# Kernel optimization log

Hardware: AMD Instinct MI355X
Metric: run time of the kernel (lower is better)

The kernel has to match this reference:

```python
import jax, jax.numpy as jnp
import numpy as np

B, DIM, HEADS = 8, 1024, 8
DH = DIM // HEADS            # 128 = dim_head
MFEAT = 621                  # int(DH * log(DH)) performer features
MAXD = 4                     # max_rel_dist
IMG = 10                     # image side; source hardcodes stride 10 in scatter indices
L = IMG * IMG + 1            # geometry forces L = img_dim**2 + 1


def _geometry():
    m, K = MAXD, 2 * MAXD - 1
    base = np.arange(-m + 1, m)
    dx = np.broadcast_to(np.tile(base, K), (L, K * K))
    dy = np.broadcast_to(np.repeat(base, K), (L, K * K))
    x_off = np.concatenate([np.tile(np.arange(IMG), IMG), [0]])[:, None]
    y_off = np.concatenate([np.repeat(np.arange(IMG), IMG), [IMG]])[:, None]
    x_pos, y_pos = dx + x_off, dy + y_off
    diffs = np.abs(dx) + np.abs(dy)
    valid = (x_pos >= 0) & (x_pos < IMG) & (y_pos >= 0) & (y_pos < IMG) & (diffs < m)
    diffs = np.where(valid, diffs, m)  # invalid taps point at the max-dist encoding
    rel_window = (m - 1) * IMG + (m - 1)
    # scatter positions inside the unfold window (stride 10 hardcoded in source)
    indices = np.tile(np.arange(K), K) + np.repeat(np.arange(K) * 10, K)
    return jnp.asarray(diffs), jnp.asarray(valid), jnp.asarray(indices - rel_window)

DIFFS, VALID, OFFSETS = _geometry()  # [L,K2] int, [L,K2] bool, [K2] int


def softmax_kernel(data, proj, is_query, eps=1e-4):
    dn = data.shape[-1] ** -0.25
    ratio = proj.shape[0] ** -0.5
    dd = jnp.einsum('...id,jd->...ij', data * dn, proj)
    diag = (jnp.sum(data ** 2, -1) * (0.5 * dn * dn))[..., None]
    mx = jnp.max(dd, -1, keepdims=True) if is_query else jnp.max(dd)
    return ratio * (jnp.exp(dd - diag - mx) + eps)


def relative_attention(q, rpe, v):
    # q: [b,h,L,MFEAT] kernel features, rpe: [R,MFEAT], v: [b,h,L,DH]
    mde = rpe[-1]                                   # max-distance encoding
    v_sum = v.sum(-2)                               # [b,h,DH]
    q_dot = jnp.einsum('bhlm,rm->bhlr', q, rpe - mde)
    q_rel = jnp.take_along_axis(q_dot, DIFFS[None, None], axis=-1)  # [b,h,L,K2]
    q_rel = jnp.where(VALID[None, None], q_rel, 0.0)
    # gather v at relative offsets (equivalent to the zero-padded unfold +
    # sparse scatter of q_rel in the source, without the dense 67-wide window)
    pos = jnp.arange(L)[:, None] + OFFSETS[None, :]  # [L,K2]
    inb = (pos >= 0) & (pos < L)
    v_g = v[:, :, jnp.clip(pos, 0, L - 1), :]        # [b,h,L,K2,DH]
    v_g = jnp.where(inb[None, None, :, :, None], v_g, 0.0)
    denom = (rpe[DIFFS] - mde).sum(1) + mde * L      # [L,MFEAT]
    D_inv = 1.0 / jnp.einsum('bhlm,lm->bhl', q, denom)
    q_md = jnp.einsum('bhlm,m->bhl', q, mde)
    out = jnp.einsum('bhl,bhd->bhld', q_md, v_sum) + jnp.einsum('bhlk,bhlkd->bhld', q_rel, v_g)
    return out * D_inv[..., None]


def setup_inputs() -> dict:
    key = jax.random.key(0)
    ks = jax.random.split(key, 9)
    s = DIM ** -0.5
    return {
        'x': jax.random.normal(ks[0], (B, L, DIM), jnp.float32),
        'Wq': jax.random.normal(ks[1], (DIM, DIM), jnp.float32) * s,
        'bq': jnp.zeros((DIM,), jnp.float32),
        'Wv': jax.random.normal(ks[2], (DIM, DIM), jnp.float32) * s,
        'bv': jnp.zeros((DIM,), jnp.float32),
        'rpe': jax.random.normal(ks[3], (MAXD + 1, DH), jnp.float32) * 0.02,
        'proj': jax.random.normal(ks[4], (MFEAT, DH), jnp.float32),
        'Wo': jax.random.normal(ks[5], (DIM, DIM), jnp.float32) * s,
        'bo': jnp.zeros((DIM,), jnp.float32),
    }


def reference(x, Wq, bq, Wv, bv, rpe, proj, Wo, bo):
    b = x.shape[0]
    q = (x @ Wq.T + bq).reshape(b, L, HEADS, DH).transpose(0, 2, 1, 3)
    v = (x @ Wv.T + bv).reshape(b, L, HEADS, DH).transpose(0, 2, 1, 3)
    qf = softmax_kernel(q, proj, is_query=True)
    rf = softmax_kernel(rpe[None, None], proj, is_query=False)[0, 0]
    out = relative_attention(qf, rf, v)          # [b,h,L,DH]
    out = out.transpose(0, 2, 1, 3).reshape(b, L, DIM)
    return out @ Wo.T + bo
```

## Files before the change

kernel.cpp:

```cpp
#include <hip/hip_runtime.h>
#include <math.h>

namespace {

typedef __bf16 bf16_t;
typedef bf16_t bf16x8 __attribute__((ext_vector_type(8)));
typedef bf16_t bf16x4 __attribute__((ext_vector_type(4)));
typedef float f32x4 __attribute__((ext_vector_type(4)));

constexpr int B = 8, L = 101, DIM = 1024, H = 8, DH = 128, MF = 621, MFP = 640;
constexpr int BL = B * L;
constexpr int BLP = 832;
constexpr int BH = B * H;
constexpr int RR = BL * H;

constexpr float DN    = 0.29730177875068026f;
constexpr float DN2   = 0.08838834764831845f;
constexpr float RATIO = 0.04012861672f;
constexpr float EPS   = 1e-4f;

constexpr int NX = BL * DIM / 4;
constexpr int NP = MFP * 32;
constexpr int NR = 64 * DH / 4;
constexpr int NW = DIM * DIM / 4;
constexpr int NZ = 4 * (BLP - BL) * DIM / 4;
constexpr int NTOT = NX + NP + NR + 3 * NW + NZ;

__device__ __forceinline__ f32x4 mfma16(bf16x8 a, bf16x8 b, f32x4 c) {
  return __builtin_amdgcn_mfma_f32_16x16x32_bf16(a, b, c, 0, 0, 0);
}

__device__ __forceinline__ void split2(float f, bf16_t& h, bf16_t& l) {
  h = (bf16_t)f;
  l = (bf16_t)(f - (float)h);
}

__device__ __forceinline__ void gload_lds16(const bf16_t* g, bf16_t* l) {
  __builtin_amdgcn_global_load_lds(
      (const __attribute__((address_space(1))) void*)g,
      (__attribute__((address_space(3))) void*)l, 16, 0, 0);
}

__global__ __launch_bounds__(256) void split_all(const float* __restrict__ x,
                                                 const float* __restrict__ proj,
                                                 const float* __restrict__ rpe,
                                                 const float* __restrict__ Wq,
                                                 const float* __restrict__ Wv,
                                                 const float* __restrict__ Wo,
                                                 bf16_t* __restrict__ xh, bf16_t* __restrict__ xl,
                                                 bf16_t* __restrict__ ph,
                                                 bf16_t* __restrict__ rh, bf16_t* __restrict__ rl,
                                                 bf16_t* __restrict__ Wh,
                                                 bf16_t* __restrict__ Woh,
                                                 bf16_t* __restrict__ qh, bf16_t* __restrict__ ql) {
  const int u = blockIdx.x * 256 + threadIdx.x;
  if (u >= NTOT) return;
  auto emit2 = [](const float* s4, float sc, bf16_t* dh, bf16_t* dl, size_t off) {
    float4 f = *(const float4*)s4;
    bf16x4 hv, lv; bf16_t h, l;
    split2(f.x * sc, h, l); hv[0] = h; lv[0] = l;
    split2(f.y * sc, h, l); hv[1] = h; lv[1] = l;
    split2(f.z * sc, h, l); hv[2] = h; lv[2] = l;
    split2(f.w * sc, h, l); hv[3] = h; lv[3] = l;
    *(bf16x4*)(dh + off) = hv;
    *(bf16x4*)(dl + off) = lv;
  };
  auto emit1 = [](const float* s4, float sc, bf16_t* dh, size_t off) {
    float4 f = *(const float4*)s4;
    bf16x4 hv;
    hv[0] = (bf16_t)(f.x * sc); hv[1] = (bf16_t)(f.y * sc);
    hv[2] = (bf16_t)(f.z * sc); hv[3] = (bf16_t)(f.w * sc);
    *(bf16x4*)(dh + off) = hv;
  };
  int t = u;
  if (t < NX) { emit2(x + (size_t)t * 4, 1.f, xh, xl, (size_t)t * 4); return; }
  t -= NX;
  if (t < NP) {
    if ((t >> 5) < MF) emit1(proj + (size_t)t * 4, DN, ph, (size_t)t * 4);
    else { bf16x4 z = {}; *(bf16x4*)(ph + (size_t)t * 4) = z; }
    return;
  }
  t -= NP;
  if (t < NR) {
    if (t < 5 * DH / 4) emit2(rpe + (size_t)t * 4, 1.f, rh, rl, (size_t)t * 4);
    else { bf16x4 z = {}; *(bf16x4*)(rh + (size_t)t * 4) = z; *(bf16x4*)(rl + (size_t)t * 4) = z; }
    return;
  }
  t -= NR;
  if (t < NW) { emit1(Wq + (size_t)t * 4, 1.f, Wh, (size_t)t * 4); return; }
  t -= NW;
  if (t < NW) { emit1(Wv + (size_t)t * 4, 1.f, Wh, (size_t)(t + NW) * 4); return; }
  t -= NW;
  if (t < NW) { emit1(Wo + (size_t)t * 4, 1.f, Woh, (size_t)t * 4); return; }
  t -= NW;
  {
    const int buf = t / 6144, o = t % 6144;
    bf16_t* dst = (buf == 0) ? xh : (buf == 1) ? xl : (buf == 2) ? qh : ql;
    bf16x4 z = {};
    *(bf16x4*)(dst + (size_t)BL * DIM + (size_t)o * 4) = z;
  }
}

template<int MODE>
__global__ __launch_bounds__(256) void gemm64(const bf16_t* __restrict__ Ah,
                                              const bf16_t* __restrict__ Al,
                                              const bf16_t* __restrict__ Bh,
                                              const float* __restrict__ bias0,
                                              const float* __restrict__ bias1,
                                              float* __restrict__ Cf,
                                              bf16_t* __restrict__ Ch,
                                              bf16_t* __restrict__ Cl) {
  constexpr int K = 1024, BK = 64, NK = K / BK;
  __shared__ bf16_t lds[2][3][64 * 64];
  const int tid = threadIdx.x;
  const int w = tid >> 6, lane = tid & 63;
  const int wr = w >> 1, wc = w & 1;
  const int l15 = lane & 15, l4 = lane >> 4;
  const int rowBase = blockIdx.y * 64, colBase = blockIdx.x * 64;
  const int r8 = lane >> 3;
  const int cs = (lane & 7) ^ r8;
  const bf16_t* src = (w == 0) ? Ah : (w == 1) ? Al : Bh;
  const int grow0 = (w < 2) ? rowBase : colBase + ((w == 3) ? 32 : 0);
  const bf16_t* srcL = src + (size_t)(grow0 + r8) * K + cs * 8;
  const int tt = (w < 2) ? w : 2;
  const int dst0 = (w == 3) ? 32 * 64 : 0;
  auto STAGE = [&](int bf, int k0) {
    if (w < 2) {
#pragma unroll
      for (int j = 0; j < 8; ++j)
        gload_lds16(srcL + (size_t)(8 * j) * K + k0, &lds[bf][tt][j * 512]);
    } else {
#pragma unroll
      for (int j = 0; j < 4; ++j)
        gload_lds16(srcL + (size_t)(8 * j) * K + k0, &lds[bf][2][dst0 + j * 512]);
    }
  };
  const int ra0 = wr * 32 + l15, ra1 = ra0 + 16;
  const int rb0 = wc * 32 + l15, rb1 = rb0 + 16;
  auto TADDR = [](int row, int kg) { return row * 64 + (((kg) ^ (row & 7)) << 3); };
  f32x4 acc[2][2] = {};
  STAGE(0, 0);
  __syncthreads();
  int bf = 0;
  for (int ks = 0; ks < NK; ++ks) {
    if (ks + 1 < NK) STAGE(bf ^ 1, (ks + 1) * BK);
#pragma unroll
    for (int subk = 0; subk < 2; ++subk) {
      const int kg = subk * 4 + l4;
      bf16x8 a0h = *(const bf16x8*)&lds[bf][0][TADDR(ra0, kg)];
      bf16x8 a0l = *(const bf16x8*)&lds[bf][1][TADDR(ra0, kg)];
      bf16x8 a1h = *(const bf16x8*)&lds[bf][0][TADDR(ra1, kg)];
      bf16x8 a1l = *(const bf16x8*)&lds[bf][1][TADDR(ra1, kg)];
      bf16x8 b0  = *(const bf16x8*)&lds[bf][2][TADDR(rb0, kg)];
      bf16x8 b1  = *(const bf16x8*)&lds[bf][2][TADDR(rb1, kg)];
      acc[0][0] = mfma16(a0h, b0, acc[0][0]);
      acc[0][0] = mfma16(a0l, b0, acc[0][0]);
      acc[0][1] = mfma16(a0h, b1, acc[0][1]);
      acc[0][1] = mfma16(a0l, b1, acc[0][1]);
      acc[1][0] = mfma16(a1h, b0, acc[1][0]);
      acc[1][0] = mfma16(a1l, b0, acc[1][0]);
      acc[1][1] = mfma16(a1h, b1, acc[1][1]);
      acc[1][1] = mfma16(a1l, b1, acc[1][1]);
    }
    __syncthreads();
    bf ^= 1;
  }
#pragma unroll
  for (int ni = 0; ni < 2; ++ni) {
    const int col = colBase + wc * 32 + ni * 16 + l15;
#pragma unroll
    for (int mi = 0; mi < 2; ++mi) {
#pragma unroll
      for (int r2 = 0; r2 < 4; ++r2) {
        const int row = rowBase + wr * 32 + mi * 16 + l4 * 4 + r2;
        if (row < BL) {
          if (MODE == 0) {
            Cf[(size_t)row * 1024 + col] = acc[mi][ni][r2] + bias0[col];
          } else {
            if (col < 1024) {
              float val = acc[mi][ni][r2] + bias0[col];
              bf16_t h, lo; split2(val, h, lo);
              Ch[(size_t)row * 1024 + col] = h;
              Cl[(size_t)row * 1024 + col] = lo;
            } else {
              Cf[(size_t)row * 1024 + (col - 1024)] = acc[mi][ni][r2] + bias1[col - 1024];
            }
          }
        }
      }
    }
  }
}

__global__ __launch_bounds__(256) void dd_gemm(const bf16_t* __restrict__ Ah,
                                               const bf16_t* __restrict__ Al,
                                               const bf16_t* __restrict__ Rh,
                                               const bf16_t* __restrict__ Rl,
                                               const bf16_t* __restrict__ Bh,
                                               float* __restrict__ dd) {
  constexpr int KK = 128, NK = 4;
  __shared__ bf16_t ldsA[2][2][32 * 32];
  __shared__ bf16_t ldsB[2][64 * 32];
  const int tid = threadIdx.x;
  const int w = tid >> 6, lane = tid & 63;
  const int wr = w >> 1, wc = w & 1;
  const int l15 = lane & 15, l4 = lane >> 4;
  int rowBase = blockIdx.y * 32;
  int outRow0 = rowBase;
  const bf16_t* Asrc_h = Ah;
  const bf16_t* Asrc_l = Al;
  if (blockIdx.y >= 202) {
    rowBase = (blockIdx.y - 202) * 32;
    outRow0 = RR + rowBase;
    Asrc_h = Rh; Asrc_l = Rl;
  }
  const int colBase = blockIdx.x * 64;
  const int r4 = lane >> 2;
  const int cs = (lane & 3) ^ (r4 & 3);
  const bf16_t* src = (w == 0) ? Asrc_h : (w == 1) ? Asrc_l : Bh;
  const int grow0 = (w < 2) ? rowBase : colBase + ((w == 3) ? 32 : 0);
  const int dstB = (w == 3) ? 1024 : 0;
  const bf16_t* srcL = src + (size_t)(grow0 + r4) * KK + cs * 8;
  auto STAGE = [&](int bf, int k0) {
    if (w < 2) {
#pragma unroll
      for (int j = 0; j < 2; ++j)
        gload_lds16(srcL + (size_t)(16 * j) * KK + k0, &ldsA[bf][w][j * 512]);
    } else {
#pragma unroll
      for (int j = 0; j < 2; ++j)
        gload_lds16(srcL + (size_t)(16 * j) * KK + k0, &ldsB[bf][dstB + j * 512]);
    }
  };
  const int cX = (l4 ^ (l15 & 3)) * 8;
  const int aoff = (wr * 16 + l15) * 32 + cX;
  const int boff0 = (wc * 32 + l15) * 32 + cX, boff1 = boff0 + 16 * 32;
  f32x4 acc[2] = {};
  STAGE(0, 0);
  __syncthreads();
  int bf = 0;
#pragma unroll
  for (int ks = 0; ks < NK; ++ks) {
    if (ks + 1 < NK) STAGE(bf ^ 1, (ks + 1) * 32);
    bf16x8 a_h = *(const bf16x8*)&ldsA[bf][0][aoff];
    bf16x8 a_l = *(const bf16x8*)&ldsA[bf][1][aoff];
    bf16x8 b0 = *(const bf16x8*)&ldsB[bf][boff0];
    bf16x8 b1 = *(const bf16x8*)&ldsB[bf][boff1];
    acc[0] = mfma16(a_h, b0, acc[0]);
    acc[0] = mfma16(a_l, b0, acc[0]);
    acc[1] = mfma16(a_h, b1, acc[1]);
    acc[1] = mfma16(a_l, b1, acc[1]);
    __syncthreads();
    bf ^= 1;
  }
#pragma unroll
  for (int ni = 0; ni < 2; ++ni) {
    const int col = colBase + wc * 32 + ni * 16 + l15;
#pragma unroll
    for (int r2 = 0; r2 < 4; ++r2) {
      const int row = outRow0 + wr * 16 + l4 * 4 + r2;
      dd[(size_t)row * MFP + col] = acc[ni][r2];
    }
  }
}

__global__ __launch_bounds__(256) void qf2_kernel(const float* __restrict__ dd,
                                                  const bf16_t* __restrict__ qh,
                                                  const bf16_t* __restrict__ ql,
                                                  const float* __restrict__ rpe,
                                                  const float* __restrict__ v,
                                                  float* __restrict__ vsum,
                                                  float* __restrict__ fd) {
  const int tid = threadIdx.x;
  if (blockIdx.x >= 808) {
    const int bi = blockIdx.x - 808;
    const int half = tid >> 7, d = tid & 127;
    const int bh = bi * 2 + half;
    const int b = bh >> 3, h = bh & 7;
    const float* base = v + (size_t)(b * L) * DIM + h * DH + d;
    float s0 = 0.f, s1 = 0.f, s2 = 0.f, s3 = 0.f;
    int l = 0;
    for (; l + 4 <= L; l += 4) {
      s0 += base[(size_t)l * DIM];
      s1 += base[(size_t)(l + 1) * DIM];
      s2 += base[(size_t)(l + 2) * DIM];
      s3 += base[(size_t)(l + 3) * DIM];
    }
    for (; l < L; ++l) s0 += base[(size_t)l * DIM];
    vsum[(size_t)bh * DH + d] = s0 + s1 + s2 + s3;
    return;
  }
  __shared__ float rfs[5][MFP];
  __shared__ float diag5v[8];
  __shared__ float redmx[4];
  const int w = tid >> 6, lane = tid & 63;
  if (tid < 40) {
    const int row = tid >> 3, ch = tid & 7;
    float s = 0.f;
#pragma unroll
    for (int e = 0; e < 16; ++e) { float f = rpe[row * DH + ch * 16 + e]; s += f * f; }
    s += __shfl_xor(s, 1, 64); s += __shfl_xor(s, 2, 64); s += __shfl_xor(s, 4, 64);
    if (ch == 0) diag5v[row] = (0.5f * DN2) * s;
  }
  float pmax = -3.4e38f;
  for (int i = tid; i < 5 * MFP; i += 256) {
    const int r = i / MFP, c = i % MFP;
    float vv = dd[(size_t)(RR + r) * MFP + c];
    rfs[r][c] = vv;
    if (c < MF) pmax = fmaxf(pmax, vv);
  }
#pragma unroll
  for (int m = 1; m <= 32; m <<= 1) pmax = fmaxf(pmax, __shfl_xor(pmax, m, 64));
  if (lane == 0) redmx[w] = pmax;
  __syncthreads();
  const float mxR = fmaxf(fmaxf(redmx[0], redmx[1]), fmaxf(redmx[2], redmx[3]));
  for (int i = tid; i < 5 * MFP; i += 256) {
    const int r = i / MFP, c = i % MFP;
    rfs[r][c] = (c < MF) ? RATIO * (__expf(rfs[r][c] - diag5v[r] - mxR) + EPS) : 0.f;
  }
  __syncthreads();
  for (int i = tid; i < 4 * MFP; i += 256) rfs[i / MFP][i % MFP] -= rfs[4][i % MFP];
  __syncthreads();
  const int rbase = blockIdx.x * 8;
#pragma unroll
  for (int rr = 0; rr < 2; ++rr) {
    const int r = rbase + w * 2 + rr;
    const float* row = dd + (size_t)r * MFP;
    float vv[10];
#pragma unroll
    for (int t = 0; t < 10; ++t) vv[t] = row[lane + 64 * t];
    float m = -3.4e38f;
#pragma unroll
    for (int t = 0; t < 10; ++t) if (lane + 64 * t < MF) m = fmaxf(m, vv[t]);
#pragma unroll
    for (int mk = 1; mk <= 32; mk <<= 1) m = fmaxf(m, __shfl_xor(m, mk, 64));
    float d0 = (float)qh[(size_t)r * DH + lane] + (float)ql[(size_t)r * DH + lane];
    float d1 = (float)qh[(size_t)r * DH + 64 + lane] + (float)ql[(size_t)r * DH + 64 + lane];
    float dsq = d0 * d0 + d1 * d1;
#pragma unroll
    for (int mk = 1; mk <= 32; mk <<= 1) dsq += __shfl_xor(dsq, mk, 64);
    const float sub = (0.5f * DN2) * dsq + m;
    float s0 = 0, s1 = 0, s2 = 0, s3 = 0, s4 = 0;
#pragma unroll
    for (int t = 0; t < 10; ++t) {
      const int c = lane + 64 * t;
      const float qfv = RATIO * (__expf(vv[t] - sub) + EPS);
      s0 += qfv * rfs[0][c]; s1 += qfv * rfs[1][c]; s2 += qfv * rfs[2][c];
      s3 += qfv * rfs[3][c]; s4 += qfv * rfs[4][c];
    }
#pragma unroll
    for (int mk = 1; mk <= 32; mk <<= 1) {
      s0 += __shfl_xor(s0, mk, 64); s1 += __shfl_xor(s1, mk, 64);
      s2 += __shfl_xor(s2, mk, 64); s3 += __shfl_xor(s3, mk, 64);
      s4 += __shfl_xor(s4, mk, 64);
    }
    if (lane == 0) {
      float* f = fd + (size_t)r * 8;
      f[0] = s0; f[1] = s1; f[2] = s2; f[3] = s3; f[4] = s4;
    }
  }
}

__global__ __launch_bounds__(256) void out_kernel(const float* __restrict__ fd,
                                                  const float* __restrict__ v,
                                                  const float* __restrict__ vsum,
                                                  bf16_t* __restrict__ attnh,
                                                  bf16_t* __restrict__ attnl) {
  const int tid = threadIdx.x;
  const int sub = tid >> 7, d = tid & 127;
  const int bh = blockIdx.y, b = bh >> 3, h = bh & 7;
  const int l = blockIdx.x * 2 + sub;
  if (l >= L) return;
  const size_t r = (size_t)(b * L + l) * H + h;
  const float q0 = fd[r * 8 + 0], q1 = fd[r * 8 + 1], q2 = fd[r * 8 + 2],
              q3 = fd[r * 8 + 3], sM = fd[r * 8 + 4];
  float o = sM * vsum[(size_t)bh * DH + d];
  float c0 = 0, c1 = 0, c2 = 0, c3 = 0;
  const int xo = (l < 100) ? (l % 10) : 0;
  const int yo = (l < 100) ? (l / 10) : 10;
#pragma unroll
  for (int k = 0; k < 49; ++k) {
    const int dx = (k % 7) - 3, dy = (k / 7) - 3;
    const int xp = xo + dx, yp = yo + dy;
    const int df = (dx < 0 ? -dx : dx) + (dy < 0 ? -dy : dy);
    if (xp >= 0 && xp < 10 && yp >= 0 && yp < 10 && df < 4) {
      float qq;
      if (df == 0)      { c0 += 1.f; qq = q0; }
      else if (df == 1) { c1 += 1.f; qq = q1; }
      else if (df == 2) { c2 += 1.f; qq = q2; }
      else              { c3 += 1.f; qq = q3; }
      const int pos = l + dx + 10 * dy;
      o += qq * v[(size_t)(b * L + pos) * DIM + h * DH + d];
    }
  }
  const float D = c0 * q0 + c1 * q1 + c2 * q2 + c3 * q3 + (float)L * sM;
  const float val = o / D;
  bf16_t hi, lo; split2(val, hi, lo);
  const size_t oi = (size_t)(b * L + l) * DIM + h * DH + d;
  attnh[oi] = hi;
  attnl[oi] = lo;
}

}

extern "C" void kernel_launch(void* const* d_in, const int* in_sizes, int n_in,
                              void* d_out, int out_size, void* d_ws, size_t ws_size,
                              hipStream_t stream) {
  const float* x    = (const float*)d_in[0];
  const float* Wq   = (const float*)d_in[1];
  const float* bq   = (const float*)d_in[2];
  const float* Wv   = (const float*)d_in[3];
  const float* bv   = (const float*)d_in[4];
  const float* rpe  = (const float*)d_in[5];
  const float* proj = (const float*)d_in[6];
  const float* Wo   = (const float*)d_in[7];
  const float* bo   = (const float*)d_in[8];

  char* p = (char*)d_ws;
  auto alloc = [&](size_t bytes) { char* r = p; p += (bytes + 255) & ~255ull; return r; };
  bf16_t* xh  = (bf16_t*)alloc((size_t)BLP * DIM * 2);
  bf16_t* xl  = (bf16_t*)alloc((size_t)BLP * DIM * 2);
  bf16_t* Wh  = (bf16_t*)alloc((size_t)2 * DIM * DIM * 2);
  bf16_t* Woh = (bf16_t*)alloc((size_t)DIM * DIM * 2);
  bf16_t* ph  = (bf16_t*)alloc((size_t)MFP * DH * 2);
  bf16_t* rh  = (bf16_t*)alloc((size_t)64 * DH * 2);
  bf16_t* rl  = (bf16_t*)alloc((size_t)64 * DH * 2);
  bf16_t* qh  = (bf16_t*)alloc((size_t)BLP * DIM * 2);
  bf16_t* ql  = (bf16_t*)alloc((size_t)BLP * DIM * 2);
  float*  v   = (float*)alloc((size_t)BL * DIM * 4);
  float*  dd  = (float*)alloc((size_t)(RR + 64) * MFP * 4);
  float*  fd  = (float*)alloc((size_t)RR * 8 * 4);
  float*  vsm = (float*)alloc((size_t)BH * DH * 4);

  split_all<<<(NTOT + 255) / 256, 256, 0, stream>>>(x, proj, rpe, Wq, Wv, Wo,
                                                    xh, xl, ph, rh, rl,
                                                    Wh, Woh, qh, ql);
  gemm64<1><<<dim3(32, 13), 256, 0, stream>>>(xh, xl, Wh, bq, bv, v, qh, ql);
  dd_gemm<<<dim3(10, 204), 256, 0, stream>>>(qh, ql, rh, rl, ph, dd);
  qf2_kernel<<<808 + 32, 256, 0, stream>>>(dd, qh, ql, rpe, v, vsm, fd);
  out_kernel<<<dim3((L + 1) / 2, BH), 256, 0, stream>>>(fd, v, vsm, qh, ql);
  gemm64<0><<<dim3(16, 13), 256, 0, stream>>>(qh, ql, Woh, bo, nullptr,
                                              (float*)d_out, nullptr, nullptr);
}
```

Baseline: 85.09 us.

## Fuse projection GEMM into feature kernel, eliminating dd intermediate buffer

The separate dd_gemm kernel, which wrote a large fp32 dd matrix to global memory, is merged into the qf kernel. Each block now computes its 32 query rows and the 5 rpe rows against all projection chunks with MFMA in registers, then does the max, exp and dot reductions in place. This removes a kernel launch and the global write and re-read of dd. In exchange, every block recomputes the rpe features, the grid drops to 202 blocks, and register and LDS pressure rise, which may lower occupancy.

```diff
diff --git a/kernel.cpp b/kernel.cpp
--- a/kernel.cpp
+++ b/kernel.cpp
@@ -192,88 +192,18 @@
   }
 }
 
-__global__ __launch_bounds__(256) void dd_gemm(const bf16_t* __restrict__ Ah,
-                                               const bf16_t* __restrict__ Al,
-                                               const bf16_t* __restrict__ Rh,
-                                               const bf16_t* __restrict__ Rl,
-                                               const bf16_t* __restrict__ Bh,
-                                               float* __restrict__ dd) {
-  constexpr int KK = 128, NK = 4;
-  __shared__ bf16_t ldsA[2][2][32 * 32];
-  __shared__ bf16_t ldsB[2][64 * 32];
-  const int tid = threadIdx.x;
-  const int w = tid >> 6, lane = tid & 63;
-  const int wr = w >> 1, wc = w & 1;
-  const int l15 = lane & 15, l4 = lane >> 4;
-  int rowBase = blockIdx.y * 32;
-  int outRow0 = rowBase;
-  const bf16_t* Asrc_h = Ah;
-  const bf16_t* Asrc_l = Al;
-  if (blockIdx.y >= 202) {
-    rowBase = (blockIdx.y - 202) * 32;
-    outRow0 = RR + rowBase;
-    Asrc_h = Rh; Asrc_l = Rl;
-  }
-  const int colBase = blockIdx.x * 64;
-  const int r4 = lane >> 2;
-  const int cs = (lane & 3) ^ (r4 & 3);
-  const bf16_t* src = (w == 0) ? Asrc_h : (w == 1) ? Asrc_l : Bh;
-  const int grow0 = (w < 2) ? rowBase : colBase + ((w == 3) ? 32 : 0);
-  const int dstB = (w == 3) ? 1024 : 0;
-  const bf16_t* srcL = src + (size_t)(grow0 + r4) * KK + cs * 8;
-  auto STAGE = [&](int bf, int k0) {
-    if (w < 2) {
-#pragma unroll
-      for (int j = 0; j < 2; ++j)
-        gload_lds16(srcL + (size_t)(16 * j) * KK + k0, &ldsA[bf][w][j * 512]);
-    } else {
-#pragma unroll
-      for (int j = 0; j < 2; ++j)
-        gload_lds16(srcL + (size_t)(16 * j) * KK + k0, &ldsB[bf][dstB + j * 512]);
-    }
-  };
-  const int cX = (l4 ^ (l15 & 3)) * 8;
-  const int aoff = (wr * 16 + l15) * 32 + cX;
-  const int boff0 = (wc * 32 + l15) * 32 + cX, boff1 = boff0 + 16 * 32;
-  f32x4 acc[2] = {};
-  STAGE(0, 0);
-  __syncthreads();
-  int bf = 0;
-#pragma unroll
-  for (int ks = 0; ks < NK; ++ks) {
-    if (ks + 1 < NK) STAGE(bf ^ 1, (ks + 1) * 32);
-    bf16x8 a_h = *(const bf16x8*)&ldsA[bf][0][aoff];
-    bf16x8 a_l = *(const bf16x8*)&ldsA[bf][1][aoff];
-    bf16x8 b0 = *(const bf16x8*)&ldsB[bf][boff0];
-    bf16x8 b1 = *(const bf16x8*)&ldsB[bf][boff1];
-    acc[0] = mfma16(a_h, b0, acc[0]);
-    acc[0] = mfma16(a_l, b0, acc[0]);
-    acc[1] = mfma16(a_h, b1, acc[1]);
-    acc[1] = mfma16(a_l, b1, acc[1]);
-    __syncthreads();
-    bf ^= 1;
-  }
-#pragma unroll
-  for (int ni = 0; ni < 2; ++ni) {
-    const int col = colBase + wc * 32 + ni * 16 + l15;
-#pragma unroll
-    for (int r2 = 0; r2 < 4; ++r2) {
-      const int row = outRow0 + wr * 16 + l4 * 4 + r2;
-      dd[(size_t)row * MFP + col] = acc[ni][r2];
-    }
-  }
-}
-
-__global__ __launch_bounds__(256) void qf2_kernel(const float* __restrict__ dd,
-                                                  const bf16_t* __restrict__ qh,
+__global__ __launch_bounds__(256) void qf3_kernel(const bf16_t* __restrict__ qh,
                                                   const bf16_t* __restrict__ ql,
+                                                  const bf16_t* __restrict__ rh,
+                                                  const bf16_t* __restrict__ rl,
+                                                  const bf16_t* __restrict__ ph,
                                                   const float* __restrict__ rpe,
                                                   const float* __restrict__ v,
                                                   float* __restrict__ vsum,
                                                   float* __restrict__ fd) {
   const int tid = threadIdx.x;
-  if (blockIdx.x >= 808) {
-    const int bi = blockIdx.x - 808;
+  if (blockIdx.x >= 202) {
+    const int bi = blockIdx.x - 202;
     const int half = tid >> 7, d = tid & 127;
     const int bh = bi * 2 + half;
     const int b = bh >> 3, h = bh & 7;
@@ -290,10 +220,56 @@
     vsum[(size_t)bh * DH + d] = s0 + s1 + s2 + s3;
     return;
   }
+  __shared__ bf16_t Ahl[2][64 * 128];
+  __shared__ bf16_t Bch[2][64 * 128];
   __shared__ float rfs[5][MFP];
+  __shared__ float diag[32];
   __shared__ float diag5v[8];
-  __shared__ float redmx[4];
+  __shared__ float mxs[4][32];
+  __shared__ float mxAll[32];
+  __shared__ float mxrf[4];
+  __shared__ float sred[4][32][5];
   const int w = tid >> 6, lane = tid & 63;
+  const int l15 = lane & 15, l4 = lane >> 4;
+  const int r0 = blockIdx.x * 32;
+  const int r4 = lane >> 4;
+  const int cg = lane & 15;
+  {
+    const bf16_t* srcA = (w == 0) ? qh : (w == 1) ? ql : (w == 2) ? rh : rl;
+    const int arow0 = (w < 2) ? r0 : 0;
+    bf16_t* dstA = &Ahl[w & 1][(w >= 2 ? 32 : 0) * 128];
+    const bf16_t* peA = srcA + (size_t)(arow0 + r4) * DH + ((cg ^ r4) << 3);
+    const bf16_t* poA = srcA + (size_t)(arow0 + r4) * DH + ((cg ^ r4 ^ 4) << 3);
+#pragma unroll
+    for (int j = 0; j < 8; ++j)
+      gload_lds16(((j & 1) ? poA : peA) + (size_t)(4 * j) * DH, dstA + j * 512);
+  }
+  const bf16_t* peB = ph + (size_t)(w * 16 + r4) * DH + ((cg ^ r4) << 3);
+  const bf16_t* poB = ph + (size_t)(w * 16 + r4) * DH + ((cg ^ r4 ^ 4) << 3);
+  auto STAGE_B = [&](int buf, int c) {
+    const size_t coff = (size_t)c * 64 * DH;
+#pragma unroll
+    for (int j = 0; j < 4; ++j)
+      gload_lds16(((j & 1) ? poB : peB) + coff + (size_t)(4 * j) * DH,
+                  &Bch[buf][(w * 16 + j * 4) * 128]);
+  };
+  {
+    const int row = tid >> 3, ch = tid & 7;
+    const size_t base = (size_t)(r0 + row) * DH + ch * 16;
+    float s = 0.f;
+#pragma unroll
+    for (int t = 0; t < 2; ++t) {
+      bf16x8 vh = *(const bf16x8*)(qh + base + t * 8);
+      bf16x8 vl = *(const bf16x8*)(ql + base + t * 8);
+#pragma unroll
+      for (int e = 0; e < 8; ++e) {
+        float f = (float)vh[e] + (float)vl[e];
+        s += f * f;
+      }
+    }
+    s += __shfl_xor(s, 1, 64); s += __shfl_xor(s, 2, 64); s += __shfl_xor(s, 4, 64);
+    if (ch == 0) diag[row] = (0.5f * DN2) * s;
+  }
   if (tid < 40) {
     const int row = tid >> 3, ch = tid & 7;
     float s = 0.f;
@@ -302,62 +278,138 @@
     s += __shfl_xor(s, 1, 64); s += __shfl_xor(s, 2, 64); s += __shfl_xor(s, 4, 64);
     if (ch == 0) diag5v[row] = (0.5f * DN2) * s;
   }
-  float pmax = -3.4e38f;
-  for (int i = tid; i < 5 * MFP; i += 256) {
-    const int r = i / MFP, c = i % MFP;
-    float vv = dd[(size_t)(RR + r) * MFP + c];
-    rfs[r][c] = vv;
-    if (c < MF) pmax = fmaxf(pmax, vv);
-  }
-#pragma unroll
-  for (int m = 1; m <= 32; m <<= 1) pmax = fmaxf(pmax, __shfl_xor(pmax, m, 64));
-  if (lane == 0) redmx[w] = pmax;
-  __syncthreads();
-  const float mxR = fmaxf(fmaxf(redmx[0], redmx[1]), fmaxf(redmx[2], redmx[3]));
-  for (int i = tid; i < 5 * MFP; i += 256) {
-    const int r = i / MFP, c = i % MFP;
-    rfs[r][c] = (c < MF) ? RATIO * (__expf(rfs[r][c] - diag5v[r] - mxR) + EPS) : 0.f;
-  }
+  auto TADDR = [](int row, int kg) { return row * 128 + (((kg) ^ (row & 7)) << 3); };
+  f32x4 acc[2][10] = {};
+  f32x4 accr[10] = {};
+  STAGE_B(0, 0);
+  __syncthreads();
+  int buf = 0;
+#pragma unroll
+  for (int c = 0; c < 10; ++c) {
+    if (c + 1 < 10) STAGE_B(buf ^ 1, c + 1);
+#pragma unroll
+    for (int ks = 0; ks < 4; ++ks) {
+      const int kg = ks * 4 + l4;
+      bf16x8 a0h = *(const bf16x8*)&Ahl[0][TADDR(l15, kg)];
+      bf16x8 a0l = *(const bf16x8*)&Ahl[1][TADDR(l15, kg)];
+      bf16x8 a1h = *(const bf16x8*)&Ahl[0][TADDR(16 + l15, kg)];
+      bf16x8 a1l = *(const bf16x8*)&Ahl[1][TADDR(16 + l15, kg)];
+      bf16x8 arh = *(const bf16x8*)&Ahl[0][TADDR(32 + l15, kg)];
+      bf16x8 arl = *(const bf16x8*)&Ahl[1][TADDR(32 + l15, kg)];
+      bf16x8 bb  = *(const bf16x8*)&Bch[buf][TADDR(w * 16 + l15, kg)];
+      acc[0][c] = mfma16(a0h, bb, acc[0][c]);
+      acc[0][c] = mfma16(a0l, bb, acc[0][c]);
+      acc[1][c] = mfma16(a1h, bb, acc[1][c]);
+      acc[1][c] = mfma16(a1l, bb, acc[1][c]);
+      accr[c]   = mfma16(arh, bb, accr[c]);
+      accr[c]   = mfma16(arl, bb, accr[c]);
+    }
+    __syncthreads();
+    buf ^= 1;
+  }
+  float pm[2][4];
+#pragma unroll
+  for (int mi = 0; mi < 2; ++mi)
+#pragma unroll
+    for (int r2 = 0; r2 < 4; ++r2) {
+      float m = -3.4e38f;
+#pragma unroll
+      for (int ni = 0; ni < 10; ++ni) {
+        const int col = ni * 64 + w * 16 + l15;
+        float vv = (col < MF) ? acc[mi][ni][r2] : -3.4e38f;
+        m = fmaxf(m, vv);
+      }
+      pm[mi][r2] = m;
+    }
+#pragma unroll
+  for (int mask = 1; mask <= 8; mask <<= 1)
+#pragma unroll
+    for (int mi = 0; mi < 2; ++mi)
+#pragma unroll
+      for (int r2 = 0; r2 < 4; ++r2)
+        pm[mi][r2] = fmaxf(pm[mi][r2], __shfl_xor(pm[mi][r2], mask, 64));
+  if (l15 == 0) {
+#pragma unroll
+    for (int mi = 0; mi < 2; ++mi)
+#pragma unroll
+      for (int r2 = 0; r2 < 4; ++r2)
+        mxs[w][mi * 16 + l4 * 4 + r2] = pm[mi][r2];
+  }
+  {
+    float m = -3.4e38f;
+#pragma unroll
+    for (int ni = 0; ni < 10; ++ni) {
+      const int col = ni * 64 + w * 16 + l15;
+#pragma unroll
+      for (int r2 = 0; r2 < 4; ++r2) {
+        const int row5 = l4 * 4 + r2;
+        if (row5 < 5 && col < MF) m = fmaxf(m, accr[ni][r2]);
+      }
+    }
+#pragma unroll
+    for (int mask = 1; mask <= 32; mask <<= 1) m = fmaxf(m, __shfl_xor(m, mask, 64));
+    if (lane == 0) mxrf[w] = m;
+  }
+  __syncthreads();
+  {
+    const float mxR = fmaxf(fmaxf(mxrf[0], mxrf[1]), fmaxf(mxrf[2], mxrf[3]));
+#pragma unroll
+    for (int ni = 0; ni < 10; ++ni) {
+      const int col = ni * 64 + w * 16 + l15;
+#pragma unroll
+      for (int r2 = 0; r2 < 4; ++r2) {
+        const int row5 = l4 * 4 + r2;
+        if (row5 < 5) {
+          float val = (col < MF)
+              ? RATIO * (__expf(accr[ni][r2] - diag5v[row5] - mxR) + EPS) : 0.f;
+          rfs[row5][col] = val;
+        }
+      }
+    }
+  }
+  if (tid < 32)
+    mxAll[tid] = fmaxf(fmaxf(mxs[0][tid], mxs[1][tid]), fmaxf(mxs[2][tid], mxs[3][tid]));
   __syncthreads();
   for (int i = tid; i < 4 * MFP; i += 256) rfs[i / MFP][i % MFP] -= rfs[4][i % MFP];
   __syncthreads();
-  const int rbase = blockIdx.x * 8;
-#pragma unroll
-  for (int rr = 0; rr < 2; ++rr) {
-    const int r = rbase + w * 2 + rr;
-    const float* row = dd + (size_t)r * MFP;
-    float vv[10];
-#pragma unroll
-    for (int t = 0; t < 10; ++t) vv[t] = row[lane + 64 * t];
-    float m = -3.4e38f;
-#pragma unroll
-    for (int t = 0; t < 10; ++t) if (lane + 64 * t < MF) m = fmaxf(m, vv[t]);
-#pragma unroll
-    for (int mk = 1; mk <= 32; mk <<= 1) m = fmaxf(m, __shfl_xor(m, mk, 64));
-    float d0 = (float)qh[(size_t)r * DH + lane] + (float)ql[(size_t)r * DH + lane];
-    float d1 = (float)qh[(size_t)r * DH + 64 + lane] + (float)ql[(size_t)r * DH + 64 + lane];
-    float dsq = d0 * d0 + d1 * d1;
-#pragma unroll
-    for (int mk = 1; mk <= 32; mk <<= 1) dsq += __shfl_xor(dsq, mk, 64);
-    const float sub = (0.5f * DN2) * dsq + m;
-    float s0 = 0, s1 = 0, s2 = 0, s3 = 0, s4 = 0;
-#pragma unroll
-    for (int t = 0; t < 10; ++t) {
-      const int c = lane + 64 * t;
-      const float qfv = RATIO * (__expf(vv[t] - sub) + EPS);
-      s0 += qfv * rfs[0][c]; s1 += qfv * rfs[1][c]; s2 += qfv * rfs[2][c];
-      s3 += qfv * rfs[3][c]; s4 += qfv * rfs[4][c];
-    }
-#pragma unroll
-    for (int mk = 1; mk <= 32; mk <<= 1) {
-      s0 += __shfl_xor(s0, mk, 64); s1 += __shfl_xor(s1, mk, 64);
-      s2 += __shfl_xor(s2, mk, 64); s3 += __shfl_xor(s3, mk, 64);
-      s4 += __shfl_xor(s4, mk, 64);
-    }
-    if (lane == 0) {
-      float* f = fd + (size_t)r * 8;
-      f[0] = s0; f[1] = s1; f[2] = s2; f[3] = s3; f[4] = s4;
-    }
+  float s[2][4][5] = {};
+#pragma unroll
+  for (int mi = 0; mi < 2; ++mi)
+#pragma unroll
+    for (int r2 = 0; r2 < 4; ++r2) {
+      const int row = mi * 16 + l4 * 4 + r2;
+      const float sub = diag[row] + mxAll[row];
+#pragma unroll
+      for (int ni = 0; ni < 10; ++ni) {
+        const int col = ni * 64 + w * 16 + l15;
+        const float qfv = RATIO * (__expf(acc[mi][ni][r2] - sub) + EPS);
+#pragma unroll
+        for (int c = 0; c < 5; ++c) s[mi][r2][c] += qfv * rfs[c][col];
+      }
+    }
+#pragma unroll
+  for (int mask = 1; mask <= 8; mask <<= 1)
+#pragma unroll
+    for (int mi = 0; mi < 2; ++mi)
+#pragma unroll
+      for (int r2 = 0; r2 < 4; ++r2)
+#pragma unroll
+        for (int c = 0; c < 5; ++c)
+          s[mi][r2][c] += __shfl_xor(s[mi][r2][c], mask, 64);
+  if (l15 == 0) {
+#pragma unroll
+    for (int mi = 0; mi < 2; ++mi)
+#pragma unroll
+      for (int r2 = 0; r2 < 4; ++r2)
+#pragma unroll
+        for (int c = 0; c < 5; ++c)
+          sred[w][mi * 16 + l4 * 4 + r2][c] = s[mi][r2][c];
+  }
+  __syncthreads();
+  if (tid < 160) {
+    const int row = tid / 5, c = tid % 5;
+    fd[(size_t)(r0 + row) * 8 + c] =
+        sred[0][row][c] + sred[1][row][c] + sred[2][row][c] + sred[3][row][c];
   }
 }
 
@@ -428,7 +480,6 @@
   bf16_t* qh  = (bf16_t*)alloc((size_t)BLP * DIM * 2);
   bf16_t* ql  = (bf16_t*)alloc((size_t)BLP * DIM * 2);
   float*  v   = (float*)alloc((size_t)BL * DIM * 4);
-  float*  dd  = (float*)alloc((size_t)(RR + 64) * MFP * 4);
   float*  fd  = (float*)alloc((size_t)RR * 8 * 4);
   float*  vsm = (float*)alloc((size_t)BH * DH * 4);
 
@@ -436,8 +487,7 @@
                                                     xh, xl, ph, rh, rl,
                                                     Wh, Woh, qh, ql);
   gemm64<1><<<dim3(32, 13), 256, 0, stream>>>(xh, xl, Wh, bq, bv, v, qh, ql);
-  dd_gemm<<<dim3(10, 204), 256, 0, stream>>>(qh, ql, rh, rl, ph, dd);
-  qf2_kernel<<<808 + 32, 256, 0, stream>>>(dd, qh, ql, rpe, v, vsm, fd);
+  qf3_kernel<<<202 + 32, 256, 0, stream>>>(qh, ql, rh, rl, ph, rpe, v, vsm, fd);
   out_kernel<<<dim3((L + 1) / 2, BH), 256, 0, stream>>>(fd, v, vsm, qh, ql);
   gemm64<0><<<dim3(16, 13), 256, 0, stream>>>(qh, ql, Woh, bo, nullptr,
                                               (float*)d_out, nullptr, nullptr);
```

After: 76.95 us. 9.6% less time.
